# Performance work log

Hardware: AMD Instinct MI355X
Metric: run time of the kernel (lower is better)

Reference implementation:

```python
import jax, jax.numpy as jnp
import numpy as np

N_P = 100000   # number of platforms (rows of pF)
N_M = 100000   # number of modules (rows of M)
R = 64         # embedding rank r = M.shape[1]
S = 3          # number of interference terms s
B = 500000     # batch of (i, j, k) index triples
ALPHA = 0.001
BETA = 0.001


def setup_inputs() -> dict:
    key = jax.random.key(0)
    k1, k2, k3 = jax.random.split(key, 3)
    pF = jax.random.normal(k1, (N_P, R * (1 + 2 * S)), dtype=jnp.float32)
    M = jax.random.normal(k2, (N_M, R), dtype=jnp.float32)
    ijk = jax.random.randint(k3, (B, 3), 0, N_M)  # i,j,k indices; k==-1 would mask
    return {"pF": pF, "M": M, "ijk": ijk}


def reference(pF, M, ijk):
    # MatrixFactorizationIF.__call__ with baseline=None, full=False, log=True.
    r = M.shape[1]
    i, j, k = ijk[:, 0], ijk[:, 1], ijk[:, 2]
    pFi = pF[i]                                        # [B, r*(1+2s)] gather
    Pi = pFi[:, :r]                                    # [B, r]
    Vs = BETA * pFi[:, r:(1 + S) * r].reshape(-1, r, S)  # [B, r, s]
    Vg = BETA * pFi[:, (1 + S) * r:].reshape(-1, r, S)   # [B, r, s]
    Mj = M[j]                                          # [B, r]
    kc = jnp.where(k < 0, 0, k)                        # clamp invalid k for gather
    Mk = M[kc]                                         # [B, r]
    mask = (k != -1).astype(M.dtype)                   # 1[valid k]
    a = jnp.einsum('brs,br->bs', Vs, Mj)               # V_s[i]^T m_j
    g = jnp.einsum('brs,br->bs', Vg, Mk)               # V_g[i]^T m_k
    mFm = mask * jnp.sum(a * g, axis=-1)               # interference term
    return ALPHA * jnp.sum(Pi * Mj, axis=-1) + mFm     # C_bar = 0 (no baseline)
```

## Files before the change

### kernel.cpp

```cpp
#include <hip/hip_runtime.h>

constexpr float ALPHA = 0.001f;
constexpr float BETA  = 0.001f;
constexpr int R   = 64;
constexpr int S   = 3;
constexpr int PFW = R * (1 + 2 * S);
constexpr int BSH  = 7;
constexpr int MAXB = 800;
constexpr int SBLK = 256;

__device__ __forceinline__ float bfhi(unsigned u) {
    union { unsigned u; float f; } c; c.u = u & 0xffff0000u; return c.f;
}
__device__ __forceinline__ float bflo(unsigned u) {
    union { unsigned u; float f; } c; c.u = u << 16; return c.f;
}

__global__ __launch_bounds__(256) void hist_kernel(const int* __restrict__ ijk, int B,
                                                   int chunk, int nb, int* __restrict__ hist) {
    __shared__ int lh[MAXB];
    for (int t = threadIdx.x; t < nb; t += blockDim.x) lh[t] = 0;
    __syncthreads();
    const int lo = blockIdx.x * chunk, hi = min(B, lo + chunk);
    for (int idx = lo + threadIdx.x; idx < hi; idx += blockDim.x)
        atomicAdd(&lh[ijk[3 * idx] >> BSH], 1);
    __syncthreads();
    for (int t = threadIdx.x; t < nb; t += blockDim.x)
        if (lh[t]) atomicAdd(&hist[t], lh[t]);
}

__global__ __launch_bounds__(1024) void scan_kernel(const int* __restrict__ hist,
                                                    int* __restrict__ cursor, int nb) {
    __shared__ int buf[1024];
    int t = threadIdx.x;
    int own = (t < nb) ? hist[t] : 0;
    buf[t] = own;
    __syncthreads();
    for (int d = 1; d < 1024; d <<= 1) {
        int v = (t >= d) ? buf[t - d] : 0;
        __syncthreads();
        buf[t] += v;
        __syncthreads();
    }
    if (t < nb) cursor[t] = buf[t] - own;
}

__global__ __launch_bounds__(256) void scatconv_kernel(
    const int* __restrict__ ijk, int B, int chunk, int nb,
    int* __restrict__ cursor, int4* __restrict__ sorted,
    const float* __restrict__ M, uint4* __restrict__ Mb, int n8)
{
    if (blockIdx.x >= SBLK) {
        const int idx = (blockIdx.x - SBLK) * 256 + threadIdx.x;
        if (idx < n8) {
            const float* src = M + (size_t)idx * 8;
            unsigned w[8];
            #pragma unroll
            for (int t = 0; t < 8; ++t) {
                union { float f; unsigned u; } c;
                c.f = __builtin_nontemporal_load(src + t);
                w[t] = (c.u + 0x7fffu + ((c.u >> 16) & 1u)) >> 16;
            }
            Mb[idx] = make_uint4(w[0] | (w[1] << 16), w[2] | (w[3] << 16),
                                 w[4] | (w[5] << 16), w[6] | (w[7] << 16));
        }
        return;
    }
    __shared__ int cnt[MAXB];
    __shared__ int base[MAXB];
    __shared__ int rnk[MAXB];
    for (int t = threadIdx.x; t < nb; t += blockDim.x) { cnt[t] = 0; rnk[t] = 0; }
    __syncthreads();
    const int lo = blockIdx.x * chunk, hi = min(B, lo + chunk);
    for (int idx = lo + threadIdx.x; idx < hi; idx += blockDim.x)
        atomicAdd(&cnt[ijk[3 * idx] >> BSH], 1);
    __syncthreads();
    for (int t = threadIdx.x; t < nb; t += blockDim.x)
        if (cnt[t]) base[t] = atomicAdd(&cursor[t], cnt[t]);
    __syncthreads();
    for (int idx = lo + threadIdx.x; idx < hi; idx += blockDim.x) {
        const int i = ijk[3 * idx], j = ijk[3 * idx + 1], k = ijk[3 * idx + 2];
        const int bkt = i >> BSH;
        const int p = base[bkt] + atomicAdd(&rnk[bkt], 1);
        sorted[p] = make_int4(i, j, k, idx);
    }
}

__global__ __launch_bounds__(256) void mfc_kernel(
    const float* __restrict__ pF,
    const uint2* __restrict__ Mb,
    const int4*  __restrict__ sorted,
    float* __restrict__ out,
    int B, int nwg)
{
    __shared__ float MjS[16][64];
    __shared__ float MkS[16][64];

    const int orig = blockIdx.x;
    const int q = nwg >> 3, r = nwg & 7;
    const int xcd = orig & 7;
    const int wgid = (xcd < r ? xcd * (q + 1) : r * (q + 1) + (xcd - r) * q) + (orig >> 3);

    const int sub = threadIdx.x & 15;
    const int g   = threadIdx.x >> 4;
    const long pos0 = (long)wgid * 16 + g;
    const bool act = pos0 < B;
    const long pos = act ? pos0 : (long)(B - 1);

    const int4 s = sorted[pos];
    const int kc = (s.z < 0) ? 0 : s.z;

    const uint2 uj = Mb[(size_t)s.y * 16 + sub];
    const uint2 uk = Mb[(size_t)kc  * 16 + sub];
    const float4 mjv = make_float4(bflo(uj.x), bfhi(uj.x), bflo(uj.y), bfhi(uj.y));
    const float4 mkv = make_float4(bflo(uk.x), bfhi(uk.x), bflo(uk.y), bfhi(uk.y));

    const float4* pFi = reinterpret_cast<const float4*>(pF + (size_t)s.x * PFW);
    const float4 pi = pFi[sub];
    const float4 vA = pFi[16 + sub], vB = pFi[32 + sub], vC = pFi[48 + sub];
    const float4 wA = pFi[64 + sub], wB = pFi[80 + sub], wC = pFi[96 + sub];

    *reinterpret_cast<float4*>(&MjS[g][4 * sub]) = mjv;
    *reinterpret_cast<float4*>(&MkS[g][4 * sub]) = mkv;
    __syncthreads();

    const int rA = (4 * sub) / 3;          const int eA = sub % 3;
    const int rB = 21 + (4 * sub + 1) / 3; const int eB = (sub + 1) % 3;
    const int rC = 42 + (4 * sub + 2) / 3; const int eC = (sub + 2) % 3;

    const float mA0 = MjS[g][rA], mA1 = MjS[g][rA + 1];
    const float mB0 = MjS[g][rB], mB1 = MjS[g][rB + 1];
    const float mC0 = MjS[g][rC], mC1 = MjS[g][rC + 1];
    const float nA0 = MkS[g][rA], nA1 = MkS[g][rA + 1];
    const float nB0 = MkS[g][rB], nB1 = MkS[g][rB + 1];
    const float nC0 = MkS[g][rC], nC1 = MkS[g][rC + 1];

    float p = pi.x * mjv.x + pi.y * mjv.y + pi.z * mjv.z + pi.w * mjv.w;

    float ah0 = vA.x * mA0 + vA.w * mA1;
    float ah1 = vA.y * (eA >= 2 ? mA1 : mA0);
    float ah2 = vA.z * (eA >= 1 ? mA1 : mA0);
    ah1 += vB.x * mB0 + vB.w * mB1;
    ah2 += vB.y * (eB >= 2 ? mB1 : mB0);
    ah0 += vB.z * (eB >= 1 ? mB1 : mB0);
    ah2 += vC.x * mC0 + vC.w * mC1;
    ah0 += vC.y * (eC >= 2 ? mC1 : mC0);
    ah1 += vC.z * (eC >= 1 ? mC1 : mC0);

    float gh0 = wA.x * nA0 + wA.w * nA1;
    float gh1 = wA.y * (eA >= 2 ? nA1 : nA0);
    float gh2 = wA.z * (eA >= 1 ? nA1 : nA0);
    gh1 += wB.x * nB0 + wB.w * nB1;
    gh2 += wB.y * (eB >= 2 ? nB1 : nB0);
    gh0 += wB.z * (eB >= 1 ? nB1 : nB0);
    gh2 += wC.x * nC0 + wC.w * nC1;
    gh0 += wC.y * (eC >= 2 ? nC1 : nC0);
    gh1 += wC.z * (eC >= 1 ? nC1 : nC0);

    const int sg = sub % 3;
    float a0 = sg == 0 ? ah0 : (sg == 1 ? ah2 : ah1);
    float a1 = sg == 0 ? ah1 : (sg == 1 ? ah0 : ah2);
    float a2 = sg == 0 ? ah2 : (sg == 1 ? ah1 : ah0);

    #pragma unroll
    for (int off = 8; off >= 1; off >>= 1) {
        p  += __shfl_xor(p,  off);
        a0 += __shfl_xor(a0, off);
        a1 += __shfl_xor(a1, off);
        a2 += __shfl_xor(a2, off);
    }
    const float ar0 = sg == 0 ? a0 : (sg == 1 ? a1 : a2);
    const float ar1 = sg == 0 ? a1 : (sg == 1 ? a2 : a0);
    const float ar2 = sg == 0 ? a2 : (sg == 1 ? a0 : a1);
    float h = ar0 * gh0 + ar1 * gh1 + ar2 * gh2;
    #pragma unroll
    for (int off = 8; off >= 1; off >>= 1)
        h += __shfl_xor(h, off);

    if (act && sub == 0) {
        const float mfm = (s.z != -1) ? (BETA * BETA) * h : 0.0f;
        out[s.w] = ALPHA * p + mfm;
    }
}

__global__ __launch_bounds__(256) void mf_if_kernel(
    const float* __restrict__ pF,
    const float* __restrict__ M,
    const int*   __restrict__ ijk,
    float* __restrict__ out,
    int B)
{
    const int sub = threadIdx.x & 15;
    const long pos = (long)blockIdx.x * 16 + (threadIdx.x >> 4);
    if (pos >= B) return;

    const int i = ijk[3 * pos], j = ijk[3 * pos + 1], k = ijk[3 * pos + 2];
    const int kc = (k < 0) ? 0 : k;

    const float4* pFi = reinterpret_cast<const float4*>(pF + (size_t)i * PFW);
    const float4 mj = reinterpret_cast<const float4*>(M + (size_t)j  * R)[sub];
    const float4 mk = reinterpret_cast<const float4*>(M + (size_t)kc * R)[sub];

    const float4 pi = pFi[sub];
    float p = pi.x * mj.x + pi.y * mj.y + pi.z * mj.z + pi.w * mj.w;
    const float4 v0 = pFi[16 + 3 * sub], v1 = pFi[17 + 3 * sub], v2 = pFi[18 + 3 * sub];
    float a0 = v0.x * mj.x + v0.w * mj.y + v1.z * mj.z + v2.y * mj.w;
    float a1 = v0.y * mj.x + v1.x * mj.y + v1.w * mj.z + v2.z * mj.w;
    float a2 = v0.z * mj.x + v1.y * mj.y + v2.x * mj.z + v2.w * mj.w;
    const float4 w0 = pFi[64 + 3 * sub], w1 = pFi[65 + 3 * sub], w2 = pFi[66 + 3 * sub];
    float g0 = w0.x * mk.x + w0.w * mk.y + w1.z * mk.z + w2.y * mk.w;
    float g1 = w0.y * mk.x + w1.x * mk.y + w1.w * mk.z + w2.z * mk.w;
    float g2 = w0.z * mk.x + w1.y * mk.y + w2.x * mk.z + w2.w * mk.w;

    #pragma unroll
    for (int off = 8; off >= 1; off >>= 1) {
        p  += __shfl_xor(p,  off);
        a0 += __shfl_xor(a0, off); a1 += __shfl_xor(a1, off); a2 += __shfl_xor(a2, off);
        g0 += __shfl_xor(g0, off); g1 += __shfl_xor(g1, off); g2 += __shfl_xor(g2, off);
    }
    if (sub == 0) {
        const float mfm = (k != -1) ? (BETA * BETA) * (a0 * g0 + a1 * g1 + a2 * g2) : 0.0f;
        out[pos] = ALPHA * p + mfm;
    }
}

extern "C" void kernel_launch(void* const* d_in, const int* in_sizes, int n_in,
                              void* d_out, int out_size, void* d_ws, size_t ws_size,
                              hipStream_t stream) {
    const float* pF  = (const float*)d_in[0];
    const float* M   = (const float*)d_in[1];
    const int*   ijk = (const int*)d_in[2];
    float* out = (float*)d_out;

    const int B   = in_sizes[2] / 3;
    const int N_P = in_sizes[0] / PFW;
    const int N_M = in_sizes[1] / R;
    const int nb  = (N_P + (1 << BSH) - 1) >> BSH;

    const size_t sorted_off = 16 * 1024;
    const size_t mb_off     = sorted_off + (size_t)B * sizeof(int4);
    const size_t need_full  = mb_off + (size_t)N_M * R * 2;

    if (nb <= MAXB && ws_size >= need_full) {
        int*   hist   = (int*)d_ws;
        int*   cursor = (int*)((char*)d_ws + 4096);
        int4*  sorted = (int4*)((char*)d_ws + sorted_off);
        uint4* Mb     = (uint4*)((char*)d_ws + mb_off);
        const int chunk = (B + SBLK - 1) / SBLK;
        const int n8 = N_M * R / 8;
        const int convBlocks = (n8 + 255) / 256;

        hipMemsetAsync(d_ws, 0, 8192, stream);
        hist_kernel<<<SBLK, 256, 0, stream>>>(ijk, B, chunk, nb, hist);
        scan_kernel<<<1, 1024, 0, stream>>>(hist, cursor, nb);
        scatconv_kernel<<<SBLK + convBlocks, 256, 0, stream>>>(
            ijk, B, chunk, nb, cursor, sorted, M, Mb, n8);

        const int nwg = (B + 15) / 16;
        mfc_kernel<<<nwg, 256, 0, stream>>>(pF, (const uint2*)Mb, sorted, out, B, nwg);
    } else {
        mf_if_kernel<<<(B + 15) / 16, 256, 0, stream>>>(pF, M, ijk, out, B);
    }
}
```

Measured before the change: 91.29 us.

## Drop bf16 M conversion, replace memset+atomics with per-block histogram, stage sorted entries in LDS

The pass that converted M to bf16 is removed, and the main kernel now reads fp32 M rows directly. That saves a full read and write of M each call but doubles the bytes gathered per M row. The global-atomic histogram and the memset are replaced by per-block histogram rows, which a single-block kernel sums before the scan. The main kernel loads its 16 sorted entries cooperatively into LDS, and the P and interference reductions are merged into one shuffle reduction.

```diff
diff --git a/kernel.cpp b/kernel.cpp
--- a/kernel.cpp
+++ b/kernel.cpp
@@ -9,15 +9,8 @@
 constexpr int MAXB = 800;
 constexpr int SBLK = 256;
 
-__device__ __forceinline__ float bfhi(unsigned u) {
-    union { unsigned u; float f; } c; c.u = u & 0xffff0000u; return c.f;
-}
-__device__ __forceinline__ float bflo(unsigned u) {
-    union { unsigned u; float f; } c; c.u = u << 16; return c.f;
-}
-
 __global__ __launch_bounds__(256) void hist_kernel(const int* __restrict__ ijk, int B,
-                                                   int chunk, int nb, int* __restrict__ hist) {
+                                                   int chunk, int nb, int* __restrict__ ghist) {
     __shared__ int lh[MAXB];
     for (int t = threadIdx.x; t < nb; t += blockDim.x) lh[t] = 0;
     __syncthreads();
@@ -26,14 +19,19 @@
         atomicAdd(&lh[ijk[3 * idx] >> BSH], 1);
     __syncthreads();
     for (int t = threadIdx.x; t < nb; t += blockDim.x)
-        if (lh[t]) atomicAdd(&hist[t], lh[t]);
-}
-
-__global__ __launch_bounds__(1024) void scan_kernel(const int* __restrict__ hist,
-                                                    int* __restrict__ cursor, int nb) {
+        ghist[t * SBLK + blockIdx.x] = lh[t];
+}
+
+__global__ __launch_bounds__(1024) void sumscan_kernel(const int* __restrict__ ghist,
+                                                       int* __restrict__ cursor, int nb) {
     __shared__ int buf[1024];
-    int t = threadIdx.x;
-    int own = (t < nb) ? hist[t] : 0;
+    const int t = threadIdx.x;
+    int own = 0;
+    if (t < nb) {
+        const int* p = ghist + t * SBLK;
+        #pragma unroll 8
+        for (int b = 0; b < SBLK; ++b) own += p[b];
+    }
     buf[t] = own;
     __syncthreads();
     for (int d = 1; d < 1024; d <<= 1) {
@@ -45,27 +43,10 @@
     if (t < nb) cursor[t] = buf[t] - own;
 }
 
-__global__ __launch_bounds__(256) void scatconv_kernel(
-    const int* __restrict__ ijk, int B, int chunk, int nb,
-    int* __restrict__ cursor, int4* __restrict__ sorted,
-    const float* __restrict__ M, uint4* __restrict__ Mb, int n8)
-{
-    if (blockIdx.x >= SBLK) {
-        const int idx = (blockIdx.x - SBLK) * 256 + threadIdx.x;
-        if (idx < n8) {
-            const float* src = M + (size_t)idx * 8;
-            unsigned w[8];
-            #pragma unroll
-            for (int t = 0; t < 8; ++t) {
-                union { float f; unsigned u; } c;
-                c.f = __builtin_nontemporal_load(src + t);
-                w[t] = (c.u + 0x7fffu + ((c.u >> 16) & 1u)) >> 16;
-            }
-            Mb[idx] = make_uint4(w[0] | (w[1] << 16), w[2] | (w[3] << 16),
-                                 w[4] | (w[5] << 16), w[6] | (w[7] << 16));
-        }
-        return;
-    }
+__global__ __launch_bounds__(256) void scatter_kernel(const int* __restrict__ ijk, int B,
+                                                      int chunk, int nb,
+                                                      int* __restrict__ cursor,
+                                                      int4* __restrict__ sorted) {
     __shared__ int cnt[MAXB];
     __shared__ int base[MAXB];
     __shared__ int rnk[MAXB];
@@ -88,11 +69,12 @@
 
 __global__ __launch_bounds__(256) void mfc_kernel(
     const float* __restrict__ pF,
-    const uint2* __restrict__ Mb,
+    const float* __restrict__ M,
     const int4*  __restrict__ sorted,
     float* __restrict__ out,
     int B, int nwg)
 {
+    __shared__ int4  ents[16];
     __shared__ float MjS[16][64];
     __shared__ float MkS[16][64];
 
@@ -103,17 +85,24 @@
 
     const int sub = threadIdx.x & 15;
     const int g   = threadIdx.x >> 4;
+
+    if (threadIdx.x < 64) {
+        const int* sp = reinterpret_cast<const int*>(sorted);
+        long idx = (long)wgid * 64 + threadIdx.x;
+        const long mx = (long)B * 4 - 1;
+        if (idx > mx) idx = mx;
+        reinterpret_cast<int*>(ents)[threadIdx.x] = sp[idx];
+    }
+    __syncthreads();
+
     const long pos0 = (long)wgid * 16 + g;
     const bool act = pos0 < B;
-    const long pos = act ? pos0 : (long)(B - 1);
-
-    const int4 s = sorted[pos];
+    int4 s = ents[g];
+    if (!act) s = make_int4(0, 0, 0, 0);
     const int kc = (s.z < 0) ? 0 : s.z;
 
-    const uint2 uj = Mb[(size_t)s.y * 16 + sub];
-    const uint2 uk = Mb[(size_t)kc  * 16 + sub];
-    const float4 mjv = make_float4(bflo(uj.x), bfhi(uj.x), bflo(uj.y), bfhi(uj.y));
-    const float4 mkv = make_float4(bflo(uk.x), bfhi(uk.x), bflo(uk.y), bfhi(uk.y));
+    const float4 mjv = reinterpret_cast<const float4*>(M + (size_t)s.y * R)[sub];
+    const float4 mkv = reinterpret_cast<const float4*>(M + (size_t)kc  * R)[sub];
 
     const float4* pFi = reinterpret_cast<const float4*>(pF + (size_t)s.x * PFW);
     const float4 pi = pFi[sub];
@@ -164,7 +153,6 @@
 
     #pragma unroll
     for (int off = 8; off >= 1; off >>= 1) {
-        p  += __shfl_xor(p,  off);
         a0 += __shfl_xor(a0, off);
         a1 += __shfl_xor(a1, off);
         a2 += __shfl_xor(a2, off);
@@ -173,14 +161,14 @@
     const float ar1 = sg == 0 ? a1 : (sg == 1 ? a2 : a0);
     const float ar2 = sg == 0 ? a2 : (sg == 1 ? a0 : a1);
     float h = ar0 * gh0 + ar1 * gh1 + ar2 * gh2;
+    if (s.z == -1) h = 0.0f;
+
+    float z = ALPHA * p + (BETA * BETA) * h;
     #pragma unroll
     for (int off = 8; off >= 1; off >>= 1)
-        h += __shfl_xor(h, off);
-
-    if (act && sub == 0) {
-        const float mfm = (s.z != -1) ? (BETA * BETA) * h : 0.0f;
-        out[s.w] = ALPHA * p + mfm;
-    }
+        z += __shfl_xor(z, off);
+
+    if (act && sub == 0) out[s.w] = z;
 }
 
 __global__ __launch_bounds__(256) void mf_if_kernel(
@@ -234,30 +222,24 @@
 
     const int B   = in_sizes[2] / 3;
     const int N_P = in_sizes[0] / PFW;
-    const int N_M = in_sizes[1] / R;
     const int nb  = (N_P + (1 << BSH) - 1) >> BSH;
 
-    const size_t sorted_off = 16 * 1024;
-    const size_t mb_off     = sorted_off + (size_t)B * sizeof(int4);
-    const size_t need_full  = mb_off + (size_t)N_M * R * 2;
+    const size_t ghist_off  = 16 * 1024;
+    const size_t sorted_off = ghist_off + (size_t)MAXB * SBLK * sizeof(int) + 4096;
+    const size_t need_full  = sorted_off + (size_t)B * sizeof(int4);
 
     if (nb <= MAXB && ws_size >= need_full) {
-        int*   hist   = (int*)d_ws;
-        int*   cursor = (int*)((char*)d_ws + 4096);
-        int4*  sorted = (int4*)((char*)d_ws + sorted_off);
-        uint4* Mb     = (uint4*)((char*)d_ws + mb_off);
+        int*  cursor = (int*)d_ws;
+        int*  ghist  = (int*)((char*)d_ws + ghist_off);
+        int4* sorted = (int4*)((char*)d_ws + sorted_off);
         const int chunk = (B + SBLK - 1) / SBLK;
-        const int n8 = N_M * R / 8;
-        const int convBlocks = (n8 + 255) / 256;
-
-        hipMemsetAsync(d_ws, 0, 8192, stream);
-        hist_kernel<<<SBLK, 256, 0, stream>>>(ijk, B, chunk, nb, hist);
-        scan_kernel<<<1, 1024, 0, stream>>>(hist, cursor, nb);
-        scatconv_kernel<<<SBLK + convBlocks, 256, 0, stream>>>(
-            ijk, B, chunk, nb, cursor, sorted, M, Mb, n8);
+
+        hist_kernel<<<SBLK, 256, 0, stream>>>(ijk, B, chunk, nb, ghist);
+        sumscan_kernel<<<1, 1024, 0, stream>>>(ghist, cursor, nb);
+        scatter_kernel<<<SBLK, 256, 0, stream>>>(ijk, B, chunk, nb, cursor, sorted);
 
         const int nwg = (B + 15) / 16;
-        mfc_kernel<<<nwg, 256, 0, stream>>>(pF, (const uint2*)Mb, sorted, out, B, nwg);
+        mfc_kernel<<<nwg, 256, 0, stream>>>(pF, M, sorted, out, B, nwg);
     } else {
         mf_if_kernel<<<(B + 15) / 16, 256, 0, stream>>>(pF, M, ijk, out, B);
     }
```

Result: slower. 115.4 us (+26.4%).
